# Kernel optimization log

Measured on AMD Instinct MI355X. Metric: run time of the kernel, lower is better.

Reference implementation:

```python
import jax, jax.numpy as jnp
import numpy as np
from jax import lax

BN_EPS = 1e-5
PAD = ((2, 3), (1, 2))  # 'same' padding for kernel (6,4): H pad 5 -> (2,3), W pad 3 -> (1,2)
DN = ('NCHW', 'OIHW', 'NCHW')


def _conv_block(x, w, b, g, bt, m, v, pool):
    # pool(bn(relu(conv(pad(x))))) as in the torch module (eval-mode BN)
    x = lax.conv_general_dilated(x, w, (1, 1), PAD, dimension_numbers=DN)
    x = jax.nn.relu(x + b[None, :, None, None])
    scale = g / jnp.sqrt(v + BN_EPS)
    x = (x - m[None, :, None, None]) * scale[None, :, None, None] + bt[None, :, None, None]
    win = (1, 1) + pool
    return lax.reduce_window(x, -jnp.inf, lax.max, win, win, 'VALID')


def _fc_bn(x, w, b, g, bt, m, v):
    x = jax.nn.relu(x @ w.T + b)
    return (x - m) * (g / jnp.sqrt(v + BN_EPS)) + bt


def _apply_cnn(x, p):
    x = x[:, None, :, :]  # [N,1,72,64]
    x = _conv_block(x, p['conv1_w'], p['conv1_b'], p['bnc1_g'], p['bnc1_b'], p['bnc1_m'], p['bnc1_v'], (2, 2))
    x = _conv_block(x, p['conv2_w'], p['conv2_b'], p['bnc2_g'], p['bnc2_b'], p['bnc2_m'], p['bnc2_v'], (2, 2))
    x = _conv_block(x, p['conv3_w'], p['conv3_b'], p['bnc3_g'], p['bnc3_b'], p['bnc3_m'], p['bnc3_v'], (3, 4))
    x = x.reshape(x.shape[0], 6 * 4 * 64)  # NCHW contiguous flatten matches torch .view
    x = _fc_bn(x, p['fc1_w'], p['fc1_b'], p['bnf1_g'], p['bnf1_b'], p['bnf1_m'], p['bnf1_v'])
    x = _fc_bn(x, p['fc2_w'], p['fc2_b'], p['bnf2_g'], p['bnf2_b'], p['bnf2_m'], p['bnf2_v'])
    x = _fc_bn(x, p['fc3_w'], p['fc3_b'], p['bnf3_g'], p['bnf3_b'], p['bnf3_m'], p['bnf3_v'])
    # F.normalize(x, p=2, dim=1) with eps=1e-12
    nrm = jnp.linalg.norm(x, axis=1, keepdims=True)
    return x / jnp.maximum(nrm, 1e-12)


def _ssm(embeds):
    # pairwise L2 distances via Gram trick (replaces the O(n^2) python loop)
    sq = jnp.sum(embeds * embeds, axis=1)  # [n]
    d2 = sq[:, None] + sq[None, :] - 2.0 * (embeds @ embeds.T)
    dist = jnp.sqrt(jnp.maximum(d2, 1e-12))
    dist = jnp.where(d2 > 0, dist, 0.0)  # exact zeros on diagonal, nan-safe grad
    return dist / jnp.max(dist)


def setup_inputs() -> dict:
    key = jax.random.key(0)
    ks = iter(jax.random.split(key, 64))
    d = {'x': jax.random.normal(next(ks), (512, 72, 64), jnp.float32)}

    def nrm(shape, s=0.05):
        return jax.random.normal(next(ks), shape, jnp.float32) * s

    def add_bn(name, c):
        d[name + '_g'] = 1.0 + nrm((c,))
        d[name + '_b'] = nrm((c,))
        d[name + '_m'] = nrm((c,), 0.1)
        d[name + '_v'] = 0.5 + jax.random.uniform(next(ks), (c,), jnp.float32)

    d['conv1_w'] = nrm((16, 1, 6, 4), 0.2);  d['conv1_b'] = nrm((16,));  add_bn('bnc1', 16)
    d['conv2_w'] = nrm((32, 16, 6, 4), 0.1); d['conv2_b'] = nrm((32,));  add_bn('bnc2', 32)
    d['conv3_w'] = nrm((64, 32, 6, 4), 0.05); d['conv3_b'] = nrm((64,)); add_bn('bnc3', 64)
    d['fc1_w'] = nrm((512, 1536), 0.03); d['fc1_b'] = nrm((512,)); add_bn('bnf1', 512)
    d['fc2_w'] = nrm((256, 512), 0.05);  d['fc2_b'] = nrm((256,)); add_bn('bnf2', 256)
    d['fc3_w'] = nrm((128, 256), 0.07);  d['fc3_b'] = nrm((128,)); add_bn('bnf3', 128)
    return d


def reference(x,
              conv1_w, conv1_b, bnc1_g, bnc1_b, bnc1_m, bnc1_v,
              conv2_w, conv2_b, bnc2_g, bnc2_b, bnc2_m, bnc2_v,
              conv3_w, conv3_b, bnc3_g, bnc3_b, bnc3_m, bnc3_v,
              fc1_w, fc1_b, bnf1_g, bnf1_b, bnf1_m, bnf1_v,
              fc2_w, fc2_b, bnf2_g, bnf2_b, bnf2_m, bnf2_v,
              fc3_w, fc3_b, bnf3_g, bnf3_b, bnf3_m, bnf3_v):
    p = dict(conv1_w=conv1_w, conv1_b=conv1_b, bnc1_g=bnc1_g, bnc1_b=bnc1_b, bnc1_m=bnc1_m, bnc1_v=bnc1_v,
             conv2_w=conv2_w, conv2_b=conv2_b, bnc2_g=bnc2_g, bnc2_b=bnc2_b, bnc2_m=bnc2_m, bnc2_v=bnc2_v,
             conv3_w=conv3_w, conv3_b=conv3_b, bnc3_g=bnc3_g, bnc3_b=bnc3_b, bnc3_m=bnc3_m, bnc3_v=bnc3_v,
             fc1_w=fc1_w, fc1_b=fc1_b, bnf1_g=bnf1_g, bnf1_b=bnf1_b, bnf1_m=bnf1_m, bnf1_v=bnf1_v,
             fc2_w=fc2_w, fc2_b=fc2_b, bnf2_g=bnf2_g, bnf2_b=bnf2_b, bnf2_m=bnf2_m, bnf2_v=bnf2_v,
             fc3_w=fc3_w, fc3_b=fc3_b, bnf3_g=bnf3_g, bnf3_b=bnf3_b, bnf3_m=bnf3_m, bnf3_v=bnf3_v)
    embeds = _apply_cnn(x, p)  # [n, 128], L2-normalized
    return _ssm(embeds)        # [n, n]
```

## Files before the change

### kernel.cpp

```cpp
#include <hip/hip_runtime.h>
#include <hip/hip_bf16.h>
#include <math.h>


#define BN_EPS 1e-5f

typedef __attribute__((ext_vector_type(8))) short short8;
typedef __attribute__((ext_vector_type(4))) float f32x4;

__device__ __forceinline__ unsigned short f2bf(float f) {
    unsigned u = __float_as_uint(f);
    u += 0x7fffu + ((u >> 16) & 1u);
    return (unsigned short)(u >> 16);
}

__device__ __forceinline__ unsigned pkbf(float a, float b) {
    __hip_bfloat162 h = __float22bfloat162_rn(make_float2(a, b));
    return *reinterpret_cast<unsigned*>(&h);
}

__device__ __forceinline__ int sw2(int c, int h) {
    return c * 32 + ((h ^ (c & 3) ^ ((c >> 2) & 3)) << 3);
}

__global__ __launch_bounds__(256) void repack_k(
    const float* __restrict__ w1, const float* __restrict__ w2,
    const float* __restrict__ w3,
    unsigned short* __restrict__ wT1b,
    unsigned short* __restrict__ wT2b, unsigned short* __restrict__ wT3b,
    unsigned* __restrict__ mxslot)
{
    int t = blockIdx.x * 256 + threadIdx.x;
    if (t == 0) *mxslot = 0u;
    if (t < 512) {
        int k = t & 31, oc = t >> 5;
        wT1b[t] = (k < 24) ? f2bf(w1[oc * 24 + k]) : (unsigned short)0;
    }
    if (t < 12288) {
        int k = t & 31, oc = (t >> 5) & 31, kk = t >> 10;
        int ky = kk >> 1, kxp = kk & 1;
        int hi = k >> 4, ic = k & 15;
        int kx = 2 * kxp + hi;
        wT2b[t] = f2bf(w2[((oc * 16 + ic) * 6 + ky) * 4 + kx]);
    }
    if (t < 49152) {
        int ic = t & 31, oc = (t >> 5) & 63, kk = t >> 11;
        int ky = kk >> 2, kx = kk & 3;
        wT3b[t] = f2bf(w3[((oc * 32 + ic) * 6 + ky) * 4 + kx]);
    }
}

__global__ __launch_bounds__(384) void conv_all(
    const float* __restrict__ x, const unsigned short* __restrict__ wT1,
    const unsigned short* __restrict__ wT2, const unsigned short* __restrict__ wT3,
    const float* __restrict__ c1b, const float* __restrict__ g1,
    const float* __restrict__ b1, const float* __restrict__ m1,
    const float* __restrict__ v1,
    const float* __restrict__ c2b, const float* __restrict__ g2,
    const float* __restrict__ b2, const float* __restrict__ m2,
    const float* __restrict__ v2,
    const float* __restrict__ c3b, const float* __restrict__ g3,
    const float* __restrict__ b3, const float* __restrict__ m3,
    const float* __restrict__ v3,
    unsigned short* __restrict__ out3)
{
    __shared__ __align__(16) unsigned short s_out1[41 * 36 * 16];
    __shared__ __align__(16) unsigned short s_un[24 * 20 * 32];
    const int tid = threadIdx.x, nl = blockIdx.x;
    const int lane = tid & 63, wave = tid >> 6;
    const int n = lane & 15, q = lane >> 4;
    unsigned short* pa = s_un;
    unsigned short* pb = s_un + 5372;

    {
        unsigned* z32 = (unsigned*)s_un;
        for (int i = tid; i < 5372; i += 384) z32[i] = 0u;
        uint4 z4; z4.x = z4.y = z4.z = z4.w = 0u;
        for (int pc = tid; pc < 324; pc += 384) {
            int row, colc;
            if (pc < 180) { row = pc / 36; colc = pc % 36; if (row >= 2) row += 36; }
            else { int pz = pc - 180; row = 2 + (pz >> 2); colc = (pz & 3) ? 32 + (pz & 3) : 0; }
            uint4* d = (uint4*)(s_out1 + ((size_t)row * 36 + colc) * 16);
            d[0] = z4; d[1] = z4;
        }
    }
    __syncthreads();
    {
        const float4* src = (const float4*)(x + (size_t)nl * 4608);
        for (int i = tid; i < 1152; i += 384) {
            float4 val = src[i];
            int f = i * 4, row = (f >> 6) + 2, c = (f & 63) + 1;
            unsigned short h0 = f2bf(val.x), h1 = f2bf(val.y);
            unsigned short h2 = f2bf(val.z), h3 = f2bf(val.w);
            unsigned short* ap = pa + row * 68 + c;
            ap[0] = h0; ap[1] = h1; ap[2] = h2; ap[3] = h3;
            unsigned* bp = (unsigned*)(pb + row * 68 + c + 1);
            bp[0] = (unsigned)h0 | ((unsigned)h1 << 16);
            bp[1] = (unsigned)h2 | ((unsigned)h3 << 16);
        }
    }
    const float sc1 = g1[n] * rsqrtf(v1[n] + BN_EPS);
    const float bb1 = c1b[n];
    const float mm1 = b1[n] - m1[n] * sc1;
    const short8 bfr1 = *(const short8*)(wT1 + n * 32 + q * 8);
    __syncthreads();

    for (int i = 0; i < 48; ++i) {
        int t = wave * 48 + i;
        int pooled = 4 * t + (n >> 2);
        int ph = pooled >> 5, pw = pooled & 31;
        int py = (n >> 1) & 1, px = n & 1;
        int oh = 2 * ph + py, ow = 2 * pw + px;
        int r0 = (oh + 2 * q) * 68;
        const unsigned* base = px ? (const unsigned*)(pb + r0 + ow + 1)
                                  : (const unsigned*)(pa + r0 + ow);
        uint4 uu;
        uu.x = base[0];  uu.y = base[1];
        uu.z = base[34]; uu.w = base[35];
        short8 afr = *reinterpret_cast<short8*>(&uu);
        f32x4 acc = (f32x4){0.f, 0.f, 0.f, 0.f};
        acc = __builtin_amdgcn_mfma_f32_16x16x32_bf16(afr, bfr1, acc, 0, 0, 0);
        int po = 4 * t + q, oph = po >> 5, opw = po & 31;
        float mx = fmaxf(fmaxf(acc[0], acc[1]), fmaxf(acc[2], acc[3]));
        float val = fmaxf(mx + bb1, 0.f) * sc1 + mm1;
        s_out1[((oph + 2) * 36 + (opw + 1)) * 16 + n] = f2bf(val);
    }
    __syncthreads();
    {
        uint4 z4; z4.x = z4.y = z4.z = z4.w = 0u;
        for (int pc = tid; pc < 192; pc += 384) {
            int row, colc;
            if (pc < 120) { row = pc / 20; colc = pc % 20; if (row >= 2) row += 18; }
            else { int pz = pc - 120; row = 2 + (pz >> 2); colc = (pz & 3) ? 16 + (pz & 3) : 0; }
            uint4* d = (uint4*)(s_un + ((size_t)row * 20 + colc) * 32);
            d[0] = z4; d[1] = z4; d[2] = z4; d[3] = z4;
        }
    }
    float bnb2[2], bns2[2], bnm2[2];
#pragma unroll
    for (int nt = 0; nt < 2; ++nt) {
        int oc = nt * 16 + n;
        float sc = g2[oc] * rsqrtf(v2[oc] + BN_EPS);
        bnb2[nt] = c2b[oc]; bns2[nt] = sc; bnm2[nt] = b2[oc] - m2[oc] * sc;
    }
    __syncthreads();

    for (int pp = wave; pp < 36; pp += 6) {
        int ph = pp >> 1, half = pp & 1;
        f32x4 acc[2][2];
#pragma unroll
        for (int ab = 0; ab < 2; ++ab)
#pragma unroll
            for (int nt = 0; nt < 2; ++nt) acc[ab][nt] = (f32x4){0.f, 0.f, 0.f, 0.f};
#pragma unroll
        for (int ky = 0; ky < 6; ++ky)
#pragma unroll
            for (int kxp = 0; kxp < 2; ++kxp) {
                int kk = ky * 2 + kxp;
                short8 w0 = *(const short8*)(wT2 + ((size_t)(kk * 32 + n) * 32) + q * 8);
                short8 w1 = *(const short8*)(wT2 + ((size_t)(kk * 32 + 16 + n) * 32) + q * 8);
                int col = half * 16 + n + 2 * kxp;
#pragma unroll
                for (int ab = 0; ab < 2; ++ab) {
                    int row = 2 * ph + ab + ky;
                    short8 afr = *(const short8*)(s_out1 + ((size_t)(row * 36 + col) * 16) + q * 8);
                    acc[ab][0] = __builtin_amdgcn_mfma_f32_16x16x32_bf16(afr, w0, acc[ab][0], 0, 0, 0);
                    acc[ab][1] = __builtin_amdgcn_mfma_f32_16x16x32_bf16(afr, w1, acc[ab][1], 0, 0, 0);
                }
            }
        int pw0 = half * 8 + q * 2;
#pragma unroll
        for (int nt = 0; nt < 2; ++nt) {
            int oc = nt * 16 + n;
            float p0 = fmaxf(fmaxf(acc[0][nt][0], acc[0][nt][1]),
                             fmaxf(acc[1][nt][0], acc[1][nt][1]));
            float p1 = fmaxf(fmaxf(acc[0][nt][2], acc[0][nt][3]),
                             fmaxf(acc[1][nt][2], acc[1][nt][3]));
            p0 = fmaxf(p0 + bnb2[nt], 0.f) * bns2[nt] + bnm2[nt];
            p1 = fmaxf(p1 + bnb2[nt], 0.f) * bns2[nt] + bnm2[nt];
            int c1 = (ph + 2) * 20 + (pw0 + 1);
            s_un[sw2(c1, oc >> 3) + (oc & 7)] = f2bf(p0);
            s_un[sw2(c1 + 1, oc >> 3) + (oc & 7)] = f2bf(p1);
        }
    }
    __syncthreads();

    for (int u = wave; u < 24; u += 6) {
        int pr = u >> 2, nt4 = u & 3;
        f32x4 acc[3];
#pragma unroll
        for (int r = 0; r < 3; ++r) acc[r] = (f32x4){0.f, 0.f, 0.f, 0.f};
#pragma unroll
        for (int ky = 0; ky < 6; ++ky)
#pragma unroll
            for (int kx = 0; kx < 4; ++kx) {
                int kk = ky * 4 + kx;
                short8 w0 = *(const short8*)(wT3 + ((size_t)(kk * 64 + nt4 * 16 + n) * 32) + q * 8);
#pragma unroll
                for (int r = 0; r < 3; ++r) {
                    int row = 3 * pr + r + ky;
                    int c = row * 20 + n + kx;
                    short8 afr = *(const short8*)(s_un + sw2(c, q));
                    acc[r] = __builtin_amdgcn_mfma_f32_16x16x32_bf16(afr, w0, acc[r], 0, 0, 0);
                }
            }
        int oc = nt4 * 16 + n;
        float sc = g3[oc] * rsqrtf(v3[oc] + BN_EPS);
        float mx = -3.4e38f;
#pragma unroll
        for (int r = 0; r < 3; ++r)
#pragma unroll
            for (int e = 0; e < 4; ++e) mx = fmaxf(mx, acc[r][e]);
        float val = fmaxf(mx + c3b[oc], 0.f) * sc + (b3[oc] - m3[oc] * sc);
        out3[(size_t)nl * 1536 + (size_t)oc * 24 + pr * 4 + q] = f2bf(val);
    }
}

__global__ __launch_bounds__(256) void fc_m(
    const unsigned short* __restrict__ A, const float* __restrict__ Wf,
    const float* __restrict__ bias, const float* __restrict__ g,
    const float* __restrict__ bt, const float* __restrict__ m,
    const float* __restrict__ v, unsigned short* __restrict__ out_b,
    int K, int N)
{
    const int tid = threadIdx.x;
    const int lane = tid & 63, wave = tid >> 6;
    const int n = lane & 15, q = lane >> 4;
    const int wr = wave >> 1, wc = wave & 1;
    const int r0 = blockIdx.y * 32 + wr * 16;
    const int c0 = blockIdx.x * 32 + wc * 16;
    const int col = c0 + n;

    float sc = g[col] * rsqrtf(v[col] + BN_EPS);
    float bb = bias[col];
    float mm = bt[col] - m[col] * sc;

    const unsigned short* Ap = A + (size_t)(r0 + n) * K + q * 8;
    const float* Bp = Wf + (size_t)col * K + q * 8;

    f32x4 acc = (f32x4){0.f, 0.f, 0.f, 0.f};
    for (int kk = 0; kk < K; kk += 64) {
        short8 a0 = *(const short8*)(Ap + kk);
        short8 a1 = *(const short8*)(Ap + kk + 32);
        float4 f0 = *(const float4*)(Bp + kk);
        float4 f1 = *(const float4*)(Bp + kk + 4);
        float4 f2 = *(const float4*)(Bp + kk + 32);
        float4 f3 = *(const float4*)(Bp + kk + 36);
        uint4 u0, u1;
        u0.x = pkbf(f0.x, f0.y); u0.y = pkbf(f0.z, f0.w);
        u0.z = pkbf(f1.x, f1.y); u0.w = pkbf(f1.z, f1.w);
        u1.x = pkbf(f2.x, f2.y); u1.y = pkbf(f2.z, f2.w);
        u1.z = pkbf(f3.x, f3.y); u1.w = pkbf(f3.z, f3.w);
        short8 b0 = *reinterpret_cast<short8*>(&u0);
        short8 b1 = *reinterpret_cast<short8*>(&u1);
        acc = __builtin_amdgcn_mfma_f32_16x16x32_bf16(a0, b0, acc, 0, 0, 0);
        acc = __builtin_amdgcn_mfma_f32_16x16x32_bf16(a1, b1, acc, 0, 0, 0);
    }
#pragma unroll
    for (int e = 0; e < 4; ++e) {
        int row = r0 + q * 4 + e;
        float val = fmaxf(acc[e] + bb, 0.f) * sc + mm;
        out_b[(size_t)row * N + col] = f2bf(val);
    }
}

__global__ __launch_bounds__(512) void fc3norm_k(
    const unsigned short* __restrict__ A, const float* __restrict__ Wf,
    const float* __restrict__ bias, const float* __restrict__ g,
    const float* __restrict__ bt, const float* __restrict__ m,
    const float* __restrict__ v,
    float* __restrict__ E, float* __restrict__ sq)
{
    __shared__ __align__(16) float z3[16 * 128];
    const int tid = threadIdx.x;
    const int lane = tid & 63, wave = tid >> 6;
    const int n = lane & 15, q = lane >> 4;
    const int r0 = blockIdx.x * 16;
    const int col = wave * 16 + n;

    float sc = g[col] * rsqrtf(v[col] + BN_EPS);
    float bb = bias[col];
    float mm = bt[col] - m[col] * sc;

    const unsigned short* Ap = A + (size_t)(r0 + n) * 256 + q * 8;
    const float* Bp = Wf + (size_t)col * 256 + q * 8;

    f32x4 acc = (f32x4){0.f, 0.f, 0.f, 0.f};
    for (int kk = 0; kk < 256; kk += 64) {
        short8 a0 = *(const short8*)(Ap + kk);
        short8 a1 = *(const short8*)(Ap + kk + 32);
        float4 f0 = *(const float4*)(Bp + kk);
        float4 f1 = *(const float4*)(Bp + kk + 4);
        float4 f2 = *(const float4*)(Bp + kk + 32);
        float4 f3 = *(const float4*)(Bp + kk + 36);
        uint4 u0, u1;
        u0.x = pkbf(f0.x, f0.y); u0.y = pkbf(f0.z, f0.w);
        u0.z = pkbf(f1.x, f1.y); u0.w = pkbf(f1.z, f1.w);
        u1.x = pkbf(f2.x, f2.y); u1.y = pkbf(f2.z, f2.w);
        u1.z = pkbf(f3.x, f3.y); u1.w = pkbf(f3.z, f3.w);
        short8 b0 = *reinterpret_cast<short8*>(&u0);
        short8 b1 = *reinterpret_cast<short8*>(&u1);
        acc = __builtin_amdgcn_mfma_f32_16x16x32_bf16(a0, b0, acc, 0, 0, 0);
        acc = __builtin_amdgcn_mfma_f32_16x16x32_bf16(a1, b1, acc, 0, 0, 0);
    }
#pragma unroll
    for (int e = 0; e < 4; ++e) {
        float val = fmaxf(acc[e] + bb, 0.f) * sc + mm;
        z3[(q * 4 + e) * 128 + col] = val;
    }
    __syncthreads();
    if (tid < 256) {
        int row_l = tid >> 4, j = tid & 15;
        float4 v0 = *(const float4*)(z3 + row_l * 128 + j * 8);
        float4 v1 = *(const float4*)(z3 + row_l * 128 + j * 8 + 4);
        float s = v0.x * v0.x + v0.y * v0.y + v0.z * v0.z + v0.w * v0.w
                + v1.x * v1.x + v1.y * v1.y + v1.z * v1.z + v1.w * v1.w;
#pragma unroll
        for (int off = 1; off < 16; off <<= 1) s += __shfl_xor(s, off, 16);
        float nn = fmaxf(sqrtf(s), 1e-12f);
        float inv = 1.f / nn;
        int row = r0 + row_l;
        float4 e0, e1;
        e0.x = v0.x * inv; e0.y = v0.y * inv; e0.z = v0.z * inv; e0.w = v0.w * inv;
        e1.x = v1.x * inv; e1.y = v1.y * inv; e1.z = v1.z * inv; e1.w = v1.w * inv;
        *(float4*)(E + (size_t)row * 128 + j * 8) = e0;
        *(float4*)(E + (size_t)row * 128 + j * 8 + 4) = e1;
        if (j == 0) sq[row] = s * inv * inv;
    }
}

__global__ __launch_bounds__(256) void dist_k(const float* __restrict__ E,
                                              const float* __restrict__ sq,
                                              float* __restrict__ D,
                                              unsigned* __restrict__ mxslot)
{
    __shared__ __align__(16) float Ei[16 * 132];
    __shared__ __align__(16) float Ej[16 * 132];
    __shared__ float red[256];
    const int tid = threadIdx.x;
    const int bi = blockIdx.y * 16, bj = blockIdx.x * 16;
    {
        int lr = tid >> 4, lc = (tid & 15) * 8;
        float4 a0 = *(const float4*)(E + (bi + lr) * 128 + lc);
        float4 a1 = *(const float4*)(E + (bi + lr) * 128 + lc + 4);
        *(float4*)(Ei + lr * 132 + lc) = a0;
        *(float4*)(Ei + lr * 132 + lc + 4) = a1;
        float4 b0 = *(const float4*)(E + (bj + lr) * 128 + lc);
        float4 b1 = *(const float4*)(E + (bj + lr) * 128 + lc + 4);
        *(float4*)(Ej + lr * 132 + lc) = b0;
        *(float4*)(Ej + lr * 132 + lc + 4) = b1;
    }
    __syncthreads();
    const int tx = tid & 15, ty = tid >> 4;
    float dot = 0.f;
#pragma unroll 4
    for (int k = 0; k < 128; k += 4) {
        float4 a = *(const float4*)(Ei + ty * 132 + k);
        float4 b = *(const float4*)(Ej + tx * 132 + k);
        dot = fmaf(a.x, b.x, dot); dot = fmaf(a.y, b.y, dot);
        dot = fmaf(a.z, b.z, dot); dot = fmaf(a.w, b.w, dot);
    }
    int i = bi + ty, j = bj + tx;
    float d2 = sq[i] + sq[j] - 2.f * dot;
    float dist = sqrtf(fmaxf(d2, 1e-12f));
    dist = (d2 > 0.f) ? dist : 0.f;
    if (i == j) dist = 0.f;
    D[i * 512 + j] = dist;
    red[tid] = dist;
    __syncthreads();
    for (int s2 = 128; s2 > 0; s2 >>= 1) {
        if (tid < s2) red[tid] = fmaxf(red[tid], red[tid + s2]);
        __syncthreads();
    }
    if (tid == 0) atomicMax(mxslot, __float_as_uint(red[0]));
}

__global__ __launch_bounds__(256) void scale_k(float* __restrict__ D,
                                               const unsigned* __restrict__ mxslot)
{
    int idx = blockIdx.x * 256 + threadIdx.x;
    float M = __uint_as_float(*mxslot);
    D[idx] = D[idx] / M;
}

extern "C" void kernel_launch(void* const* d_in, const int* in_sizes, int n_in,
                              void* d_out, int out_size, void* d_ws, size_t ws_size,
                              hipStream_t stream)
{
    (void)in_sizes; (void)n_in; (void)out_size; (void)ws_size;
    const float* x    = (const float*)d_in[0];
    const float* c1w  = (const float*)d_in[1];
    const float* c1b  = (const float*)d_in[2];
    const float* g1   = (const float*)d_in[3];
    const float* b1   = (const float*)d_in[4];
    const float* m1   = (const float*)d_in[5];
    const float* v1   = (const float*)d_in[6];
    const float* c2w  = (const float*)d_in[7];
    const float* c2b  = (const float*)d_in[8];
    const float* g2   = (const float*)d_in[9];
    const float* b2   = (const float*)d_in[10];
    const float* m2   = (const float*)d_in[11];
    const float* v2   = (const float*)d_in[12];
    const float* c3w  = (const float*)d_in[13];
    const float* c3b  = (const float*)d_in[14];
    const float* g3   = (const float*)d_in[15];
    const float* b3   = (const float*)d_in[16];
    const float* m3   = (const float*)d_in[17];
    const float* v3   = (const float*)d_in[18];
    const float* fw1  = (const float*)d_in[19];
    const float* fb1  = (const float*)d_in[20];
    const float* gf1  = (const float*)d_in[21];
    const float* bf1  = (const float*)d_in[22];
    const float* mf1  = (const float*)d_in[23];
    const float* vf1  = (const float*)d_in[24];
    const float* fw2  = (const float*)d_in[25];
    const float* fb2  = (const float*)d_in[26];
    const float* gf2  = (const float*)d_in[27];
    const float* bf2  = (const float*)d_in[28];
    const float* mf2  = (const float*)d_in[29];
    const float* vf2  = (const float*)d_in[30];
    const float* fw3  = (const float*)d_in[31];
    const float* fb3  = (const float*)d_in[32];
    const float* gf3  = (const float*)d_in[33];
    const float* bf3  = (const float*)d_in[34];
    const float* mf3  = (const float*)d_in[35];
    const float* vf3  = (const float*)d_in[36];

    float* ws = (float*)d_ws;
    float* E    = ws + 0;
    float* sq   = ws + 65536;
    unsigned* mx = (unsigned*)(ws + 66048);
    unsigned short* wT1b = (unsigned short*)(ws + 66064);
    unsigned short* wT2b = (unsigned short*)(ws + 66320);
    unsigned short* wT3b = (unsigned short*)(ws + 72464);
    unsigned short* out3b= (unsigned short*)(ws + 97040);
    unsigned short* a1b  = (unsigned short*)(ws + 490256);
    unsigned short* a2b  = (unsigned short*)(ws + 621328);

    float* out = (float*)d_out;

    repack_k<<<192, 256, 0, stream>>>(c1w, c2w, c3w, wT1b, wT2b, wT3b, mx);
    conv_all<<<512, 384, 0, stream>>>(x, wT1b, wT2b, wT3b,
                                      c1b, g1, b1, m1, v1,
                                      c2b, g2, b2, m2, v2,
                                      c3b, g3, b3, m3, v3, out3b);
    fc_m<<<dim3(16, 16), 256, 0, stream>>>(out3b, fw1, fb1, gf1, bf1, mf1, vf1,
                                           a1b, 1536, 512);
    fc_m<<<dim3(8, 16), 256, 0, stream>>>(a1b, fw2, fb2, gf2, bf2, mf2, vf2,
                                          a2b, 512, 256);
    fc3norm_k<<<32, 512, 0, stream>>>(a2b, fw3, fb3, gf3, bf3, mf3, vf3, E, sq);
    dist_k<<<dim3(32, 32), 256, 0, stream>>>(E, sq, out, mx);
    scale_k<<<1024, 256, 0, stream>>>(out, mx);
}
```

Baseline: 229.2 us.

## Widen conv_all to 8 waves, drop LDS swizzle, reuse A-fragments across two conv3 tiles

The fused conv kernel now launches 512 threads (8 waves) instead of 384 and rebalances the conv1/conv2 loops to match. Conv3 is rebuilt so each wave computes two 16-channel output tiles from every LDS A-fragment, which halves the A loads per MFMA. The XOR swizzle on the conv2 output buffer is replaced by plain linear indexing, removing the index arithmetic but possibly adding LDS bank conflicts. With 12 conv3 work items over 8 waves the load is uneven, and the larger accumulator arrays raise register pressure.

```diff
diff --git a/kernel.cpp b/kernel.cpp
--- a/kernel.cpp
+++ b/kernel.cpp
@@ -17,10 +17,6 @@
 __device__ __forceinline__ unsigned pkbf(float a, float b) {
     __hip_bfloat162 h = __float22bfloat162_rn(make_float2(a, b));
     return *reinterpret_cast<unsigned*>(&h);
-}
-
-__device__ __forceinline__ int sw2(int c, int h) {
-    return c * 32 + ((h ^ (c & 3) ^ ((c >> 2) & 3)) << 3);
 }
 
 __global__ __launch_bounds__(256) void repack_k(
@@ -50,7 +46,7 @@
     }
 }
 
-__global__ __launch_bounds__(384) void conv_all(
+__global__ __launch_bounds__(512) void conv_all(
     const float* __restrict__ x, const unsigned short* __restrict__ wT1,
     const unsigned short* __restrict__ wT2, const unsigned short* __restrict__ wT3,
     const float* __restrict__ c1b, const float* __restrict__ g1,
@@ -74,9 +70,9 @@
 
     {
         unsigned* z32 = (unsigned*)s_un;
-        for (int i = tid; i < 5372; i += 384) z32[i] = 0u;
+        for (int i = tid; i < 5372; i += 512) z32[i] = 0u;
         uint4 z4; z4.x = z4.y = z4.z = z4.w = 0u;
-        for (int pc = tid; pc < 324; pc += 384) {
+        for (int pc = tid; pc < 324; pc += 512) {
             int row, colc;
             if (pc < 180) { row = pc / 36; colc = pc % 36; if (row >= 2) row += 36; }
             else { int pz = pc - 180; row = 2 + (pz >> 2); colc = (pz & 3) ? 32 + (pz & 3) : 0; }
@@ -87,7 +83,7 @@
     __syncthreads();
     {
         const float4* src = (const float4*)(x + (size_t)nl * 4608);
-        for (int i = tid; i < 1152; i += 384) {
+        for (int i = tid; i < 1152; i += 512) {
             float4 val = src[i];
             int f = i * 4, row = (f >> 6) + 2, c = (f & 63) + 1;
             unsigned short h0 = f2bf(val.x), h1 = f2bf(val.y);
@@ -105,8 +101,8 @@
     const short8 bfr1 = *(const short8*)(wT1 + n * 32 + q * 8);
     __syncthreads();
 
-    for (int i = 0; i < 48; ++i) {
-        int t = wave * 48 + i;
+    for (int i = 0; i < 36; ++i) {
+        int t = wave * 36 + i;
         int pooled = 4 * t + (n >> 2);
         int ph = pooled >> 5, pw = pooled & 31;
         int py = (n >> 1) & 1, px = n & 1;
@@ -128,7 +124,7 @@
     __syncthreads();
     {
         uint4 z4; z4.x = z4.y = z4.z = z4.w = 0u;
-        for (int pc = tid; pc < 192; pc += 384) {
+        for (int pc = tid; pc < 192; pc += 512) {
             int row, colc;
             if (pc < 120) { row = pc / 20; colc = pc % 20; if (row >= 2) row += 18; }
             else { int pz = pc - 120; row = 2 + (pz >> 2); colc = (pz & 3) ? 16 + (pz & 3) : 0; }
@@ -145,7 +141,7 @@
     }
     __syncthreads();
 
-    for (int pp = wave; pp < 36; pp += 6) {
+    for (int pp = wave; pp < 36; pp += 8) {
         int ph = pp >> 1, half = pp & 1;
         f32x4 acc[2][2];
 #pragma unroll
@@ -178,41 +174,48 @@
                              fmaxf(acc[1][nt][2], acc[1][nt][3]));
             p0 = fmaxf(p0 + bnb2[nt], 0.f) * bns2[nt] + bnm2[nt];
             p1 = fmaxf(p1 + bnb2[nt], 0.f) * bns2[nt] + bnm2[nt];
-            int c1 = (ph + 2) * 20 + (pw0 + 1);
-            s_un[sw2(c1, oc >> 3) + (oc & 7)] = f2bf(p0);
-            s_un[sw2(c1 + 1, oc >> 3) + (oc & 7)] = f2bf(p1);
+            s_un[((size_t)(ph + 2) * 20 + (pw0 + 1)) * 32 + oc] = f2bf(p0);
+            s_un[((size_t)(ph + 2) * 20 + (pw0 + 2)) * 32 + oc] = f2bf(p1);
         }
     }
     __syncthreads();
 
-    for (int u = wave; u < 24; u += 6) {
-        int pr = u >> 2, nt4 = u & 3;
-        f32x4 acc[3];
-#pragma unroll
-        for (int r = 0; r < 3; ++r) acc[r] = (f32x4){0.f, 0.f, 0.f, 0.f};
+    for (int ch = wave; ch < 12; ch += 8) {
+        int pr = ch >> 1, nth = ch & 1;
+        f32x4 acc[3][2];
+#pragma unroll
+        for (int r = 0; r < 3; ++r)
+#pragma unroll
+            for (int t2 = 0; t2 < 2; ++t2) acc[r][t2] = (f32x4){0.f, 0.f, 0.f, 0.f};
 #pragma unroll
         for (int ky = 0; ky < 6; ++ky)
 #pragma unroll
             for (int kx = 0; kx < 4; ++kx) {
                 int kk = ky * 4 + kx;
-                short8 w0 = *(const short8*)(wT3 + ((size_t)(kk * 64 + nt4 * 16 + n) * 32) + q * 8);
+                short8 w0 = *(const short8*)(wT3 + ((size_t)(kk * 64 + nth * 32 + n) * 32) + q * 8);
+                short8 w1 = *(const short8*)(wT3 + ((size_t)(kk * 64 + nth * 32 + 16 + n) * 32) + q * 8);
 #pragma unroll
                 for (int r = 0; r < 3; ++r) {
                     int row = 3 * pr + r + ky;
-                    int c = row * 20 + n + kx;
-                    short8 afr = *(const short8*)(s_un + sw2(c, q));
-                    acc[r] = __builtin_amdgcn_mfma_f32_16x16x32_bf16(afr, w0, acc[r], 0, 0, 0);
+                    int col = n + kx;
+                    short8 afr = *(const short8*)(s_un + ((size_t)(row * 20 + col) * 32) + q * 8);
+                    acc[r][0] = __builtin_amdgcn_mfma_f32_16x16x32_bf16(afr, w0, acc[r][0], 0, 0, 0);
+                    acc[r][1] = __builtin_amdgcn_mfma_f32_16x16x32_bf16(afr, w1, acc[r][1], 0, 0, 0);
                 }
             }
-        int oc = nt4 * 16 + n;
-        float sc = g3[oc] * rsqrtf(v3[oc] + BN_EPS);
-        float mx = -3.4e38f;
-#pragma unroll
-        for (int r = 0; r < 3; ++r)
-#pragma unroll
-            for (int e = 0; e < 4; ++e) mx = fmaxf(mx, acc[r][e]);
-        float val = fmaxf(mx + c3b[oc], 0.f) * sc + (b3[oc] - m3[oc] * sc);
-        out3[(size_t)nl * 1536 + (size_t)oc * 24 + pr * 4 + q] = f2bf(val);
+        size_t ob = (size_t)nl * 1536;
+#pragma unroll
+        for (int t2 = 0; t2 < 2; ++t2) {
+            int oc = nth * 32 + t2 * 16 + n;
+            float sc = g3[oc] * rsqrtf(v3[oc] + BN_EPS);
+            float mx = -3.4e38f;
+#pragma unroll
+            for (int r = 0; r < 3; ++r)
+#pragma unroll
+                for (int e = 0; e < 4; ++e) mx = fmaxf(mx, acc[r][t2][e]);
+            float val = fmaxf(mx + c3b[oc], 0.f) * sc + (b3[oc] - m3[oc] * sc);
+            out3[ob + (size_t)oc * 24 + pr * 4 + q] = f2bf(val);
+        }
     }
 }
 
@@ -440,7 +443,7 @@
     float* out = (float*)d_out;
 
     repack_k<<<192, 256, 0, stream>>>(c1w, c2w, c3w, wT1b, wT2b, wT3b, mx);
-    conv_all<<<512, 384, 0, stream>>>(x, wT1b, wT2b, wT3b,
+    conv_all<<<512, 512, 0, stream>>>(x, wT1b, wT2b, wT3b,
                                       c1b, g1, b1, m1, v1,
                                       c2b, g2, b2, m2, v2,
                                       c3b, g3, b3, m3, v3, out3b);
```

New measurement: 223.8 us (median of 2 runs). 2.4% less time.
